# Optimization experiments

Measured on AMD Instinct MI355X. Metric: run time of the kernel, lower is better.

## Reference

```python
import jax, jax.numpy as jnp
import numpy as np

NUM_HEADS = 8

def _ln(x, w, b, eps=1e-5):
    m = x.mean(-1, keepdims=True)
    v = ((x - m) ** 2).mean(-1, keepdims=True)
    return (x - m) / jnp.sqrt(v + eps) * w + b

def _l2n(x, axis=-1, eps=1e-12):
    n = jnp.linalg.norm(x, axis=axis, keepdims=True)
    return x / jnp.maximum(n, eps)

def setup_inputs() -> dict:
    key = jax.random.key(0)
    ks = jax.random.split(key, 30)
    B, N, C, nc, t = 2, 4096, 256, 150, 3
    Hh = Ww = 64
    hid = 4 * C
    s = 0.02
    inp = {}
    inp['x'] = jax.random.normal(ks[0], (B, N, C), jnp.float32)
    inp['z'] = jax.random.normal(ks[1], (B, nc, (t + 1) * N), jnp.float32)
    inp['mem'] = jax.random.normal(ks[2], (B * t, N, C), jnp.float32)
    inp['clustering_w'] = s * jax.random.normal(ks[3], (nc, C), jnp.float32)
    inp['prompt1'] = jax.random.normal(ks[4], (nc,), jnp.float32)
    inp['tdt1'] = jnp.eye(nc, dtype=jnp.float32) + s * jax.random.normal(ks[5], (nc, nc), jnp.float32)
    inp['prompt2'] = jax.random.normal(ks[6], (nc,), jnp.float32)
    inp['tdt2'] = jnp.eye(nc, dtype=jnp.float32) + s * jax.random.normal(ks[7], (nc, nc), jnp.float32)
    inp['sim_alpha'] = jnp.ones((1,), jnp.float32)
    inp['sim_beta'] = jnp.zeros((1,), jnp.float32)
    inp['q_w'] = s * jax.random.normal(ks[8], (C, C), jnp.float32)
    inp['q_b'] = s * jax.random.normal(ks[9], (C,), jnp.float32)
    inp['k_w'] = s * jax.random.normal(ks[10], (C, C), jnp.float32)
    inp['k_b'] = s * jax.random.normal(ks[11], (C,), jnp.float32)
    inp['v_w'] = s * jax.random.normal(ks[12], (C, C), jnp.float32)
    inp['v_b'] = s * jax.random.normal(ks[13], (C,), jnp.float32)
    inp['proj_w'] = s * jax.random.normal(ks[14], (C, C), jnp.float32)
    inp['proj_b'] = s * jax.random.normal(ks[15], (C,), jnp.float32)
    inp['norm_w'] = jnp.ones((C,), jnp.float32)
    inp['norm_b'] = jnp.zeros((C,), jnp.float32)
    inp['fc1_w'] = s * jax.random.normal(ks[16], (hid, C), jnp.float32)
    inp['fc1_b'] = s * jax.random.normal(ks[17], (hid,), jnp.float32)
    inp['dw_w'] = s * jax.random.normal(ks[18], (hid, 1, 3, 3), jnp.float32)
    inp['dw_b'] = s * jax.random.normal(ks[19], (hid,), jnp.float32)
    inp['fc2_w'] = s * jax.random.normal(ks[20], (C, hid), jnp.float32)
    inp['fc2_b'] = s * jax.random.normal(ks[21], (C,), jnp.float32)
    inp['H'] = Hh
    inp['W'] = Ww
    inp['t'] = t
    return inp

def _forward(x, z, mem, clustering_w, prompt1, tdt1, prompt2, tdt2, sim_alpha, sim_beta,
             q_w, q_b, k_w, k_b, v_w, v_b, proj_w, proj_b, norm_w, norm_b,
             fc1_w, fc1_b, dw_w, dw_b, fc2_w, fc2_b, H, W, t):
    B, N, C = x.shape
    nc = clustering_w.shape[0]
    res = x
    T = t + 1
    # cat memory frames with current frame: [(B*T), N, C]
    xf = jnp.concatenate([mem.reshape(B, t, N, C), x[:, None]], axis=1).reshape(B * T, N, C)
    # clustering head: (SRPS approximated as identity) 1x1 conv dim->num_clusters
    cl = jnp.einsum('bnc,kc->bkn', xf, clustering_w)            # [(B*T), nc, N]
    cl = cl.reshape(B, T, nc, N).transpose(0, 2, 1, 3).reshape(B, nc, T * N)
    # top-down prompt modulation of z and cluster logits
    zc = z.transpose(0, 2, 1)                                   # [B, T*N, nc]
    cos = _l2n(zc, -1) @ _l2n(prompt1[None, :, None], axis=1)   # [B, T*N, 1]
    zc = (zc * jnp.clip(cos, 0.0, 1.0)) @ tdt1
    clc = cl.transpose(0, 2, 1)
    cos = _l2n(clc, -1) @ _l2n(prompt2[None, :, None], axis=1)
    clc = (clc * jnp.clip(cos, 0.0, 1.0)) @ tdt2
    cluster_x_z = ((clc + zc) * 0.5).transpose(0, 2, 1)          # [B, nc, T*N]
    # inner_center: per-frame soft assignment -> cluster centers
    center = cluster_x_z.reshape(B, nc, T, N).transpose(0, 2, 1, 3)  # [B, T, nc, N]
    assigned_results = center
    soft = jax.nn.softmax(center, axis=-1)
    cx = xf.reshape(B, T, N, C)
    cen = jnp.einsum('btkn,btnc->btkc', soft, cx)               # [B, T, nc, C]
    last, prev = cen[:, -1], cen[:, :-1]                        # [B,nc,C], [B,t,nc,C]
    dot = jnp.einsum('bkc,btkc->btk', last, prev)
    denom = jnp.maximum(jnp.linalg.norm(last, axis=-1)[:, None] * jnp.linalg.norm(prev, axis=-1), 1e-8)
    gate = jax.nn.sigmoid(sim_beta + sim_alpha * (dot / denom))  # [B, t, nc]
    C_in = last + (gate[..., None] * prev).sum(axis=1)          # [B, nc, C]
    C_in = _ln(C_in, norm_w, norm_b)
    # cross attention: tokens query cluster centers
    hd = C // NUM_HEADS
    q = (res @ q_w.T + q_b) * (1.0 / np.sqrt(hd))
    k = C_in @ k_w.T + k_b
    v = C_in @ v_w.T + v_b
    q = q.reshape(B, N, NUM_HEADS, hd).transpose(0, 2, 1, 3)
    k = k.reshape(B, nc, NUM_HEADS, hd).transpose(0, 2, 1, 3)
    v = v.reshape(B, nc, NUM_HEADS, hd).transpose(0, 2, 1, 3)
    attn = jax.nn.softmax(jnp.einsum('bhnd,bhkd->bhnk', q, k), axis=-1)
    o = jnp.einsum('bhnk,bhkd->bhnd', attn, v).transpose(0, 2, 1, 3).reshape(B, N, C)
    o = o @ proj_w.T + proj_b
    out = res + _ln(o, norm_w, norm_b)
    # MLP with depthwise conv
    h = out @ fc1_w.T + fc1_b                                   # [B, N, 4C]
    hid = h.shape[-1]
    h_img = h.transpose(0, 2, 1).reshape(B, hid, H, W)
    h_img = jax.lax.conv_general_dilated(h_img, dw_w, (1, 1), 'SAME',
                                         feature_group_count=hid,
                                         dimension_numbers=('NCHW', 'OIHW', 'NCHW'))
    h_img = h_img + dw_b[None, :, None, None]
    h = h_img.reshape(B, hid, N).transpose(0, 2, 1)
    h = jax.nn.gelu(h, approximate=False) @ fc2_w.T + fc2_b
    out = out + _ln(h, norm_w, norm_b)
    return out, cluster_x_z, assigned_results

def reference(x, z, mem, clustering_w, prompt1, tdt1, prompt2, tdt2, sim_alpha, sim_beta,
              q_w, q_b, k_w, k_b, v_w, v_b, proj_w, proj_b, norm_w, norm_b,
              fc1_w, fc1_b, dw_w, dw_b, fc2_w, fc2_b, H, W, t):
    return _forward(x, z, mem, clustering_w, prompt1, tdt1, prompt2, tdt2, sim_alpha, sim_beta,
                    q_w, q_b, k_w, k_b, v_w, v_b, proj_w, proj_b, norm_w, norm_b,
                    fc1_w, fc1_b, dw_w, dw_b, fc2_w, fc2_b, H, W, t)
```

## Files before the change

kernel.cpp:

```cpp
#include <hip/hip_runtime.h>
#include <math.h>


typedef __attribute__((ext_vector_type(8))) short bf16x8;
typedef __attribute__((ext_vector_type(4))) float f32x4;

__device__ __forceinline__ short f2b(float f) {
  union { float f; unsigned int u; } c; c.f = f;
  unsigned int r = (c.u + 0x7fffu + ((c.u >> 16) & 1u)) >> 16;
  return (short)r;
}

__device__ __forceinline__ float bred_sum(float v, float* red) {
  int tid = threadIdx.x;
  red[tid] = v; __syncthreads();
  #pragma unroll
  for (int s = 128; s > 0; s >>= 1) {
    if (tid < s) red[tid] += red[tid + s];
    __syncthreads();
  }
  float r = red[0]; __syncthreads();
  return r;
}

__global__ __launch_bounds__(256) void gemm_mfma(
    const float* __restrict__ A, const float* __restrict__ W,
    const float* __restrict__ bias, float* __restrict__ out,
    int M, int N, int K, float alpha)
{
  __shared__ __align__(16) short As[128 * 72];
  __shared__ __align__(16) short Bs[64 * 72];
  const int tid = threadIdx.x;
  const int m0 = blockIdx.x * 128;
  const int n0 = blockIdx.y * 64;
  const int wave = tid >> 6;
  const int lane = tid & 63;
  const int wm = wave & 1, wn = wave >> 1;
  const int t16 = lane & 15;
  const int k8 = (lane >> 4) * 8;

  f32x4 acc[4][2];
  #pragma unroll
  for (int i = 0; i < 4; ++i)
    #pragma unroll
    for (int j = 0; j < 2; ++j)
      acc[i][j] = (f32x4){0.f, 0.f, 0.f, 0.f};

  const int sr = tid >> 2;
  const int sk = (tid & 3) * 16;

  for (int k0 = 0; k0 < K; k0 += 64) {
    #pragma unroll
    for (int p = 0; p < 2; ++p) {
      const int row = sr + p * 64;
      const float* ap = &A[(size_t)(m0 + row) * K + k0 + sk];
      float4 v0 = *(const float4*)&ap[0];
      float4 v1 = *(const float4*)&ap[4];
      float4 v2 = *(const float4*)&ap[8];
      float4 v3 = *(const float4*)&ap[12];
      bf16x8 w0, w1;
      w0[0] = f2b(v0.x); w0[1] = f2b(v0.y); w0[2] = f2b(v0.z); w0[3] = f2b(v0.w);
      w0[4] = f2b(v1.x); w0[5] = f2b(v1.y); w0[6] = f2b(v1.z); w0[7] = f2b(v1.w);
      w1[0] = f2b(v2.x); w1[1] = f2b(v2.y); w1[2] = f2b(v2.z); w1[3] = f2b(v2.w);
      w1[4] = f2b(v3.x); w1[5] = f2b(v3.y); w1[6] = f2b(v3.z); w1[7] = f2b(v3.w);
      *(bf16x8*)&As[row * 72 + sk] = w0;
      *(bf16x8*)&As[row * 72 + sk + 8] = w1;
    }
    {
      const float* wp = &W[(size_t)(n0 + sr) * K + k0 + sk];
      float4 v0 = *(const float4*)&wp[0];
      float4 v1 = *(const float4*)&wp[4];
      float4 v2 = *(const float4*)&wp[8];
      float4 v3 = *(const float4*)&wp[12];
      bf16x8 w0, w1;
      w0[0] = f2b(v0.x); w0[1] = f2b(v0.y); w0[2] = f2b(v0.z); w0[3] = f2b(v0.w);
      w0[4] = f2b(v1.x); w0[5] = f2b(v1.y); w0[6] = f2b(v1.z); w0[7] = f2b(v1.w);
      w1[0] = f2b(v2.x); w1[1] = f2b(v2.y); w1[2] = f2b(v2.z); w1[3] = f2b(v2.w);
      w1[4] = f2b(v3.x); w1[5] = f2b(v3.y); w1[6] = f2b(v3.z); w1[7] = f2b(v3.w);
      *(bf16x8*)&Bs[sr * 72 + sk] = w0;
      *(bf16x8*)&Bs[sr * 72 + sk + 8] = w1;
    }
    __syncthreads();
    #pragma unroll
    for (int ks = 0; ks < 2; ++ks) {
      const int kofs = ks * 32 + k8;
      bf16x8 af0 = *(const bf16x8*)&As[(wm * 64 +  0 + t16) * 72 + kofs];
      bf16x8 af1 = *(const bf16x8*)&As[(wm * 64 + 16 + t16) * 72 + kofs];
      bf16x8 af2 = *(const bf16x8*)&As[(wm * 64 + 32 + t16) * 72 + kofs];
      bf16x8 af3 = *(const bf16x8*)&As[(wm * 64 + 48 + t16) * 72 + kofs];
      bf16x8 bf0 = *(const bf16x8*)&Bs[(wn * 32 +  0 + t16) * 72 + kofs];
      bf16x8 bf1 = *(const bf16x8*)&Bs[(wn * 32 + 16 + t16) * 72 + kofs];
      acc[0][0] = __builtin_amdgcn_mfma_f32_16x16x32_bf16(af0, bf0, acc[0][0], 0, 0, 0);
      acc[1][0] = __builtin_amdgcn_mfma_f32_16x16x32_bf16(af1, bf0, acc[1][0], 0, 0, 0);
      acc[2][0] = __builtin_amdgcn_mfma_f32_16x16x32_bf16(af2, bf0, acc[2][0], 0, 0, 0);
      acc[3][0] = __builtin_amdgcn_mfma_f32_16x16x32_bf16(af3, bf0, acc[3][0], 0, 0, 0);
      acc[0][1] = __builtin_amdgcn_mfma_f32_16x16x32_bf16(af0, bf1, acc[0][1], 0, 0, 0);
      acc[1][1] = __builtin_amdgcn_mfma_f32_16x16x32_bf16(af1, bf1, acc[1][1], 0, 0, 0);
      acc[2][1] = __builtin_amdgcn_mfma_f32_16x16x32_bf16(af2, bf1, acc[2][1], 0, 0, 0);
      acc[3][1] = __builtin_amdgcn_mfma_f32_16x16x32_bf16(af3, bf1, acc[3][1], 0, 0, 0);
    }
    __syncthreads();
  }
  const int r4 = (lane >> 4) * 4;
  #pragma unroll
  for (int ni = 0; ni < 2; ++ni) {
    const int gcol = n0 + wn * 32 + ni * 16 + t16;
    const float bb = bias[gcol];
    #pragma unroll
    for (int mi = 0; mi < 4; ++mi) {
      #pragma unroll
      for (int r = 0; r < 4; ++r) {
        const int gm = m0 + wm * 64 + mi * 16 + r4 + r;
        out[(size_t)gm * N + gcol] = alpha * (acc[mi][ni][r] + bb);
      }
    }
  }
}

__global__ __launch_bounds__(256) void prep_bt(
    const float* __restrict__ cw, const float* __restrict__ tdt2, const float* __restrict__ tdt1,
    short* __restrict__ cwb, short* __restrict__ TT)
{
  int idx = blockIdx.x * 256 + threadIdx.x;
  if (idx < 160 * 256) {
    int kc = idx >> 8, k = idx & 255;
    float v = (kc < 150) ? cw[kc * 256 + k] : 0.f;
    cwb[idx] = f2b(v);
  }
  if (idx < 160 * 320) {
    int kc = idx / 320, kk = idx - kc * 320;
    float t = 0.f;
    if (kc < 150) {
      if (kk < 150) t = tdt2[kk * 150 + kc];
      else if (kk >= 160 && kk < 310) t = tdt1[(kk - 160) * 150 + kc];
    }
    TT[idx] = f2b(t);
  }
}

__global__ __launch_bounds__(256) void xf_t(
    const float* __restrict__ x, const float* __restrict__ mem, short* __restrict__ xfT)
{
  __shared__ float tile[64][257];
  const int bt = blockIdx.y;
  const int n0 = blockIdx.x * 64;
  const int b = bt >> 2, ti = bt & 3;
  const float* xf = (ti < 3) ? (mem + (size_t)(b * 3 + ti) * 4096 * 256)
                             : (x + (size_t)b * 4096 * 256);
  const int tid = threadIdx.x;
  const int r = tid >> 2, cofs = (tid & 3) * 64;
  const float* src = xf + (size_t)(n0 + r) * 256 + cofs;
  #pragma unroll
  for (int i = 0; i < 16; ++i) {
    float4 v = *(const float4*)&src[i * 4];
    tile[r][cofs + i * 4 + 0] = v.x;
    tile[r][cofs + i * 4 + 1] = v.y;
    tile[r][cofs + i * 4 + 2] = v.z;
    tile[r][cofs + i * 4 + 3] = v.w;
  }
  __syncthreads();
  short* dst = xfT + ((size_t)bt * 256 + tid) * 4096 + n0;
  #pragma unroll
  for (int seg = 0; seg < 8; ++seg) {
    bf16x8 w;
    #pragma unroll
    for (int j = 0; j < 8; ++j) w[j] = f2b(tile[seg * 8 + j][tid]);
    *(bf16x8*)&dst[seg * 8] = w;
  }
}

__global__ __launch_bounds__(256) void fused_csz(
    const float* __restrict__ x, const float* __restrict__ mem, const float* __restrict__ z,
    const short* __restrict__ cwb, const short* __restrict__ TT,
    const float* __restrict__ p1, const float* __restrict__ p2,
    float* __restrict__ csz, float* __restrict__ asg)
{
  __shared__ __align__(16) short Acatile[64 * 328];
  __shared__ float p1s[160], p2s[160];
  __shared__ float sred[4][16][9];
  __shared__ float czs[64];
  const int tid = threadIdx.x;
  const int r0 = blockIdx.x * 64;
  const int b = r0 >> 14;
  const int mmg = r0 & 16383;
  const int ti = mmg >> 12, nn = mmg & 4095;
  const float* Ab = ((ti < 3) ? (mem + (size_t)(b * 3 + ti) * 4096 * 256)
                              : (x + (size_t)b * 4096 * 256)) + (size_t)nn * 256;
  const int wave = tid >> 6, lane = tid & 63;
  const int t16 = lane & 15, quad = lane >> 4, k8 = quad * 8;

  const int kr = tid >> 4, c4 = (tid & 15) * 4;
  float4 zv[10];
  #pragma unroll
  for (int it = 0; it < 10; ++it) {
    const int k = it * 16 + kr;
    zv[it] = make_float4(0.f, 0.f, 0.f, 0.f);
    if (k < 150) zv[it] = *(const float4*)&z[((size_t)b * 150 + k) * 16384 + mmg + c4];
  }
  if (tid < 160) {
    p2s[tid] = (tid < 150) ? p2[tid] : 0.f;
    p1s[tid] = (tid < 150) ? p1[tid] : 0.f;
  }

  f32x4 acc[10];
  #pragma unroll
  for (int i = 0; i < 10; ++i) acc[i] = (f32x4){0.f, 0.f, 0.f, 0.f};
  {
    const float* ap = Ab + (size_t)(wave * 16 + t16) * 256 + k8;
    const short* bp = cwb + t16 * 256 + k8;
    #pragma unroll 2
    for (int ks = 0; ks < 8; ++ks) {
      float4 v0 = *(const float4*)&ap[ks * 32];
      float4 v1 = *(const float4*)&ap[ks * 32 + 4];
      bf16x8 a;
      a[0] = f2b(v0.x); a[1] = f2b(v0.y); a[2] = f2b(v0.z); a[3] = f2b(v0.w);
      a[4] = f2b(v1.x); a[5] = f2b(v1.y); a[6] = f2b(v1.z); a[7] = f2b(v1.w);
      #pragma unroll
      for (int nf = 0; nf < 10; ++nf) {
        bf16x8 bv = *(const bf16x8*)&bp[nf * 4096 + ks * 32];
        acc[nf] = __builtin_amdgcn_mfma_f32_16x16x32_bf16(a, bv, acc[nf], 0, 0, 0);
      }
    }
  }
  __syncthreads();

  {
    float d[4] = {0.f, 0.f, 0.f, 0.f}, s[4] = {0.f, 0.f, 0.f, 0.f};
    float pn = 0.f;
    #pragma unroll
    for (int nf = 0; nf < 10; ++nf) {
      float a2 = p2s[nf * 16 + t16];
      pn += a2 * a2;
      #pragma unroll
      for (int r = 0; r < 4; ++r) {
        float v = acc[nf][r];
        d[r] = fmaf(v, a2, d[r]);
        s[r] = fmaf(v, v, s[r]);
      }
    }
    #pragma unroll
    for (int off = 1; off < 16; off <<= 1) {
      pn += __shfl_xor(pn, off);
      #pragma unroll
      for (int r = 0; r < 4; ++r) {
        d[r] += __shfl_xor(d[r], off);
        s[r] += __shfl_xor(s[r], off);
      }
    }
    const float spn = fmaxf(sqrtf(pn), 1e-12f);
    float cs[4];
    #pragma unroll
    for (int r = 0; r < 4; ++r) {
      float c = d[r] / (fmaxf(sqrtf(s[r]), 1e-12f) * spn);
      cs[r] = fminf(fmaxf(c, 0.f), 1.f);
    }
    #pragma unroll
    for (int nf = 0; nf < 10; ++nf)
      #pragma unroll
      for (int r = 0; r < 4; ++r)
        Acatile[(wave * 16 + quad * 4 + r) * 328 + nf * 16 + t16] = f2b(acc[nf][r] * cs[r]);
  }

  {
    float d[4] = {0.f, 0.f, 0.f, 0.f}, sv[4] = {0.f, 0.f, 0.f, 0.f};
    float pn = 0.f;
    #pragma unroll
    for (int it = 0; it < 10; ++it) {
      const int k = it * 16 + kr;
      const float a = p1s[k];
      d[0] = fmaf(zv[it].x, a, d[0]); d[1] = fmaf(zv[it].y, a, d[1]);
      d[2] = fmaf(zv[it].z, a, d[2]); d[3] = fmaf(zv[it].w, a, d[3]);
      sv[0] = fmaf(zv[it].x, zv[it].x, sv[0]); sv[1] = fmaf(zv[it].y, zv[it].y, sv[1]);
      sv[2] = fmaf(zv[it].z, zv[it].z, sv[2]); sv[3] = fmaf(zv[it].w, zv[it].w, sv[3]);
      pn = fmaf(a, a, pn);
    }
    #pragma unroll
    for (int off = 16; off < 64; off <<= 1) {
      pn += __shfl_xor(pn, off);
      #pragma unroll
      for (int r = 0; r < 4; ++r) {
        d[r] += __shfl_xor(d[r], off);
        sv[r] += __shfl_xor(sv[r], off);
      }
    }
    if ((lane >> 4) == 0) {
      #pragma unroll
      for (int r = 0; r < 4; ++r) {
        sred[wave][lane][r] = d[r];
        sred[wave][lane][4 + r] = sv[r];
      }
      sred[wave][lane][8] = pn;
    }
  }
  __syncthreads();
  if (tid < 64) {
    const int cg = tid >> 2, r = tid & 3;
    float dd = 0.f, ss = 0.f, pp = 0.f;
    #pragma unroll
    for (int w = 0; w < 4; ++w) {
      dd += sred[w][cg][r];
      ss += sred[w][cg][4 + r];
      pp += sred[w][cg][8];
    }
    float c = dd / (fmaxf(sqrtf(ss), 1e-12f) * fmaxf(sqrtf(pp), 1e-12f));
    czs[tid] = fminf(fmaxf(c, 0.f), 1.f);
  }
  __syncthreads();
  {
    const float cz0 = czs[c4 + 0], cz1 = czs[c4 + 1], cz2 = czs[c4 + 2], cz3 = czs[c4 + 3];
    #pragma unroll
    for (int it = 0; it < 10; ++it) {
      const int k = it * 16 + kr;
      Acatile[(c4 + 0) * 328 + 160 + k] = f2b(zv[it].x * cz0);
      Acatile[(c4 + 1) * 328 + 160 + k] = f2b(zv[it].y * cz1);
      Acatile[(c4 + 2) * 328 + 160 + k] = f2b(zv[it].z * cz2);
      Acatile[(c4 + 3) * 328 + 160 + k] = f2b(zv[it].w * cz3);
    }
  }
  __syncthreads();

  {
    const int wm = wave & 1, wn = wave >> 1;
    f32x4 c2[2][5];
    #pragma unroll
    for (int i = 0; i < 2; ++i)
      #pragma unroll
      for (int j = 0; j < 5; ++j)
        c2[i][j] = (f32x4){0.f, 0.f, 0.f, 0.f};
    const short* bp = TT + (size_t)(wn * 80 + t16) * 320 + k8;
    #pragma unroll 2
    for (int ks = 0; ks < 10; ++ks) {
      bf16x8 a0 = *(const bf16x8*)&Acatile[(wm * 32 + t16) * 328 + ks * 32 + k8];
      bf16x8 a1 = *(const bf16x8*)&Acatile[(wm * 32 + 16 + t16) * 328 + ks * 32 + k8];
      #pragma unroll
      for (int nf = 0; nf < 5; ++nf) {
        bf16x8 bv = *(const bf16x8*)&bp[nf * 5120 + ks * 32];
        c2[0][nf] = __builtin_amdgcn_mfma_f32_16x16x32_bf16(a0, bv, c2[0][nf], 0, 0, 0);
        c2[1][nf] = __builtin_amdgcn_mfma_f32_16x16x32_bf16(a1, bv, c2[1][nf], 0, 0, 0);
      }
    }
    #pragma unroll
    for (int nf = 0; nf < 5; ++nf) {
      const int kc = wn * 80 + nf * 16 + t16;
      if (kc < 150) {
        #pragma unroll
        for (int mf = 0; mf < 2; ++mf) {
          const int moff = wm * 32 + mf * 16 + quad * 4;
          float4 r4;
          r4.x = 0.5f * c2[mf][nf][0];
          r4.y = 0.5f * c2[mf][nf][1];
          r4.z = 0.5f * c2[mf][nf][2];
          r4.w = 0.5f * c2[mf][nf][3];
          *(float4*)&csz[((size_t)b * 150 + kc) * 16384 + mmg + moff] = r4;
          *(float4*)&asg[(((size_t)b * 4 + ti) * 150 + kc) * 4096 + nn + moff] = r4;
        }
      }
    }
  }
}

__global__ __launch_bounds__(256) void softmax_stats_e(
    const float* __restrict__ csz, float* __restrict__ lr_, short* __restrict__ ecsz)
{
  __shared__ float wred[8];
  const int row = blockIdx.x;
  const int bt = row / 150, k = row - bt * 150;
  const int b = bt >> 2, ti = bt & 3;
  const float* p = csz + ((size_t)b * 150 + k) * 16384 + ti * 4096;
  const int base = threadIdx.x * 16;
  float4 v[4];
  #pragma unroll
  for (int i = 0; i < 4; ++i) v[i] = *(const float4*)&p[base + i * 4];
  float mx = -1e30f;
  #pragma unroll
  for (int i = 0; i < 4; ++i)
    mx = fmaxf(mx, fmaxf(fmaxf(v[i].x, v[i].y), fmaxf(v[i].z, v[i].w)));
  #pragma unroll
  for (int off = 1; off < 64; off <<= 1) mx = fmaxf(mx, __shfl_xor(mx, off));
  const int wave = threadIdx.x >> 6, lane = threadIdx.x & 63;
  if (lane == 0) wred[wave] = mx;
  __syncthreads();
  mx = fmaxf(fmaxf(wred[0], wred[1]), fmaxf(wred[2], wred[3]));
  const float L = 1.4426950408889634f;
  float s = 0.f;
  bf16x8 e0, e1;
  #pragma unroll
  for (int i = 0; i < 2; ++i) {
    float a = exp2f((v[i].x - mx) * L);
    float bq = exp2f((v[i].y - mx) * L);
    float cq = exp2f((v[i].z - mx) * L);
    float dq = exp2f((v[i].w - mx) * L);
    s += a + bq + cq + dq;
    e0[i * 4 + 0] = f2b(a); e0[i * 4 + 1] = f2b(bq); e0[i * 4 + 2] = f2b(cq); e0[i * 4 + 3] = f2b(dq);
  }
  #pragma unroll
  for (int i = 2; i < 4; ++i) {
    float a = exp2f((v[i].x - mx) * L);
    float bq = exp2f((v[i].y - mx) * L);
    float cq = exp2f((v[i].z - mx) * L);
    float dq = exp2f((v[i].w - mx) * L);
    s += a + bq + cq + dq;
    e1[(i - 2) * 4 + 0] = f2b(a); e1[(i - 2) * 4 + 1] = f2b(bq);
    e1[(i - 2) * 4 + 2] = f2b(cq); e1[(i - 2) * 4 + 3] = f2b(dq);
  }
  #pragma unroll
  for (int off = 1; off < 64; off <<= 1) s += __shfl_xor(s, off);
  if (lane == 0) wred[4 + wave] = s;
  __syncthreads();
  short* er = ecsz + ((size_t)bt * 160 + k) * 4096 + base;
  *(bf16x8*)&er[0] = e0;
  *(bf16x8*)&er[8] = e1;
  if (threadIdx.x == 0) lr_[row] = wred[4] + wred[5] + wred[6] + wred[7];
}

__global__ __launch_bounds__(256) void gemm_cen_at(
    const short* __restrict__ ecsz, const short* __restrict__ xfT,
    float* __restrict__ cen)
{
  __shared__ __align__(16) short As[160 * 136];
  const int tid = threadIdx.x;
  const int chalf = blockIdx.x;
  const int bt = blockIdx.y;
  const int sp = blockIdx.z;
  const int n0 = sp * 128;
  const int wave = tid >> 6, lane = tid & 63;
  const int t16 = lane & 15, quad = lane >> 4, k8 = quad * 8;
  const int cbase = chalf * 128 + wave * 32;

  f32x4 acc[10][2];
  #pragma unroll
  for (int i = 0; i < 10; ++i) {
    acc[i][0] = (f32x4){0.f, 0.f, 0.f, 0.f};
    acc[i][1] = (f32x4){0.f, 0.f, 0.f, 0.f};
  }

  const short* erow = ecsz + (size_t)bt * 160 * 4096 + n0;
  #pragma unroll
  for (int p = 0; p < 10; ++p) {
    const int g = p * 256 + tid;
    const int row = g >> 4;
    const int col8 = (g & 15) * 8;
    *(bf16x8*)&As[row * 136 + col8] = *(const bf16x8*)&erow[(size_t)row * 4096 + col8];
  }
  __syncthreads();
  const short* xrow = xfT + (size_t)bt * 256 * 4096 + n0;
  #pragma unroll
  for (int kc = 0; kc < 4; ++kc) {
    bf16x8 b0 = *(const bf16x8*)&xrow[(size_t)(cbase + t16) * 4096 + kc * 32 + k8];
    bf16x8 b1 = *(const bf16x8*)&xrow[(size_t)(cbase + 16 + t16) * 4096 + kc * 32 + k8];
    #pragma unroll
    for (int mt = 0; mt < 10; ++mt) {
      bf16x8 aA = *(const bf16x8*)&As[(mt * 16 + t16) * 136 + kc * 32 + k8];
      acc[mt][0] = __builtin_amdgcn_mfma_f32_16x16x32_bf16(aA, b0, acc[mt][0], 0, 0, 0);
      acc[mt][1] = __builtin_amdgcn_mfma_f32_16x16x32_bf16(aA, b1, acc[mt][1], 0, 0, 0);
    }
  }
  #pragma unroll
  for (int mt = 0; mt < 10; ++mt) {
    #pragma unroll
    for (int r = 0; r < 4; ++r) {
      const int grow = mt * 16 + quad * 4 + r;
      if (grow < 150) {
        atomicAdd(&cen[((size_t)bt * 150 + grow) * 256 + cbase + t16], acc[mt][0][r]);
        atomicAdd(&cen[((size_t)bt * 150 + grow) * 256 + cbase + 16 + t16], acc[mt][1][r]);
      }
    }
  }
}

__global__ __launch_bounds__(256) void gate_ln(
    const float* __restrict__ cen, const float* __restrict__ lr_,
    const float* __restrict__ alpha_, const float* __restrict__ beta_,
    const float* __restrict__ nw, const float* __restrict__ nb, float* __restrict__ cin)
{
  __shared__ float red[256];
  int bk = blockIdx.x;
  int b = bk / 150, k = bk % 150;
  int c = threadIdx.x;
  const float* base = cen + ((size_t)b * 4 * 150) * 256;
  const float* lrb = lr_ + (size_t)b * 4 * 150;
  float lc  = base[((size_t)3 * 150 + k) * 256 + c] / lrb[3 * 150 + k];
  float p0  = base[((size_t)0 * 150 + k) * 256 + c] / lrb[0 * 150 + k];
  float p1v = base[((size_t)1 * 150 + k) * 256 + c] / lrb[1 * 150 + k];
  float p2v = base[((size_t)2 * 150 + k) * 256 + c] / lrb[2 * 150 + k];
  float nl = bred_sum(lc * lc, red);
  float q0 = bred_sum(p0 * p0, red);
  float q1 = bred_sum(p1v * p1v, red);
  float q2 = bred_sum(p2v * p2v, red);
  float d0 = bred_sum(lc * p0, red);
  float d1 = bred_sum(lc * p1v, red);
  float d2 = bred_sum(lc * p2v, red);
  float al = alpha_[0], be = beta_[0];
  float snl = sqrtf(nl);
  float g0 = 1.f / (1.f + expf(-(be + al * (d0 / fmaxf(snl * sqrtf(q0), 1e-8f)))));
  float g1 = 1.f / (1.f + expf(-(be + al * (d1 / fmaxf(snl * sqrtf(q1), 1e-8f)))));
  float g2 = 1.f / (1.f + expf(-(be + al * (d2 / fmaxf(snl * sqrtf(q2), 1e-8f)))));
  float ci = lc + g0 * p0 + g1 * p1v + g2 * p2v;
  float mu = bred_sum(ci, red) * (1.f / 256.f);
  float df = ci - mu;
  float var = bred_sum(df * df, red) * (1.f / 256.f);
  cin[(size_t)bk * 256 + c] = df * rsqrtf(var + 1e-5f) * nw[c] + nb[c];
}

__global__ __launch_bounds__(256) void gemm_nt(
    const float* __restrict__ A, const float* __restrict__ W,
    const float* __restrict__ bias, float* __restrict__ out,
    int M, int N, int K, float alpha)
{
  __shared__ __align__(16) float As[16][132];
  __shared__ __align__(16) float Ws[16][68];
  const int tid = threadIdx.x;
  const int m0 = blockIdx.x * 128;
  const int n0 = blockIdx.y * 64;
  const int tm = tid & 15;
  const int tn = tid >> 4;
  float acc[8][4];
  #pragma unroll
  for (int i = 0; i < 8; ++i)
    #pragma unroll
    for (int j = 0; j < 4; ++j) acc[i][j] = 0.f;

  const int lr = tid >> 2;
  const int lk = (tid & 3) * 4;

  for (int k0 = 0; k0 < K; k0 += 16) {
    #pragma unroll
    for (int p = 0; p < 2; ++p) {
      int r = lr + p * 64;
      int gm = m0 + r;
      float4 v = make_float4(0.f, 0.f, 0.f, 0.f);
      if (gm < M) v = *(const float4*)&A[(size_t)gm * K + k0 + lk];
      As[lk + 0][r] = v.x; As[lk + 1][r] = v.y; As[lk + 2][r] = v.z; As[lk + 3][r] = v.w;
    }
    {
      float4 v = *(const float4*)&W[(size_t)(n0 + lr) * K + k0 + lk];
      Ws[lk + 0][lr] = v.x; Ws[lk + 1][lr] = v.y; Ws[lk + 2][lr] = v.z; Ws[lk + 3][lr] = v.w;
    }
    __syncthreads();
    #pragma unroll
    for (int kk = 0; kk < 16; ++kk) {
      float4 a0 = *(const float4*)&As[kk][tm * 8];
      float4 a1 = *(const float4*)&As[kk][tm * 8 + 4];
      float4 w0 = *(const float4*)&Ws[kk][tn * 4];
      float av[8] = {a0.x, a0.y, a0.z, a0.w, a1.x, a1.y, a1.z, a1.w};
      float wv[4] = {w0.x, w0.y, w0.z, w0.w};
      #pragma unroll
      for (int i = 0; i < 8; ++i)
        #pragma unroll
        for (int j = 0; j < 4; ++j)
          acc[i][j] = fmaf(av[i], wv[j], acc[i][j]);
    }
    __syncthreads();
  }
  float4 bv = *(const float4*)&bias[n0 + tn * 4];
  float bb[4] = {bv.x, bv.y, bv.z, bv.w};
  #pragma unroll
  for (int i = 0; i < 8; ++i) {
    int gm = m0 + tm * 8 + i;
    if (gm >= M) continue;
    float4 r;
    r.x = alpha * (acc[i][0] + bb[0]);
    r.y = alpha * (acc[i][1] + bb[1]);
    r.z = alpha * (acc[i][2] + bb[2]);
    r.w = alpha * (acc[i][3] + bb[3]);
    *(float4*)&out[(size_t)gm * N + n0 + tn * 4] = r;
  }
}

__global__ __launch_bounds__(256) void attn_mfma(
    const float* __restrict__ q, const float* __restrict__ ks, const float* __restrict__ vs,
    float* __restrict__ o)
{
  __shared__ __align__(16) short Ps[128 * 168];
  __shared__ __align__(16) short VT[32 * 168];
  __shared__ float lrow[128];
  const int tid = threadIdx.x;
  const int bid = blockIdx.x;
  const int ntile = bid & 31;
  const int bh = bid >> 5;
  const int b = bh >> 3, h = bh & 7;
  const int n0 = ntile * 128;
  const int wave = tid >> 6, lane = tid & 63;
  const int t16 = lane & 15, quad = lane >> 4;
  const int k8 = quad * 8;
  const int wr = wave * 32;

  for (int i = tid; i < 5120; i += 256) {
    int d = i / 160, kc = i - d * 160;
    VT[d * 168 + kc] = (kc < 150) ? f2b(vs[((size_t)b * 150 + kc) * 256 + h * 32 + d]) : (short)0;
  }

  bf16x8 aQ[2];
  #pragma unroll
  for (int mt = 0; mt < 2; ++mt) {
    const float* qp = &q[((size_t)b * 4096 + n0 + wr + mt * 16 + t16) * 256 + h * 32 + k8];
    float4 v0 = *(const float4*)&qp[0];
    float4 v1 = *(const float4*)&qp[4];
    bf16x8 w;
    w[0] = f2b(v0.x); w[1] = f2b(v0.y); w[2] = f2b(v0.z); w[3] = f2b(v0.w);
    w[4] = f2b(v1.x); w[5] = f2b(v1.y); w[6] = f2b(v1.z); w[7] = f2b(v1.w);
    aQ[mt] = w;
  }

  f32x4 s[2][10];
  #pragma unroll
  for (int ct = 0; ct < 10; ++ct) {
    const int c = ct * 16 + t16;
    bf16x8 bK = {0, 0, 0, 0, 0, 0, 0, 0};
    if (c < 150) {
      const float* kp = &ks[((size_t)b * 150 + c) * 256 + h * 32 + k8];
      float4 v0 = *(const float4*)&kp[0];
      float4 v1 = *(const float4*)&kp[4];
      bK[0] = f2b(v0.x); bK[1] = f2b(v0.y); bK[2] = f2b(v0.z); bK[3] = f2b(v0.w);
      bK[4] = f2b(v1.x); bK[5] = f2b(v1.y); bK[6] = f2b(v1.z); bK[7] = f2b(v1.w);
    }
    f32x4 zero = (f32x4){0.f, 0.f, 0.f, 0.f};
    s[0][ct] = __builtin_amdgcn_mfma_f32_16x16x32_bf16(aQ[0], bK, zero, 0, 0, 0);
    s[1][ct] = __builtin_amdgcn_mfma_f32_16x16x32_bf16(aQ[1], bK, zero, 0, 0, 0);
  }

  #pragma unroll
  for (int mt = 0; mt < 2; ++mt) {
    #pragma unroll
    for (int r = 0; r < 4; ++r) {
      float mx = -1e30f;
      #pragma unroll
      for (int ct = 0; ct < 10; ++ct) {
        float v = s[mt][ct][r];
        if (ct == 9 && t16 >= 6) { v = -1e30f; s[mt][ct][r] = v; }
        mx = fmaxf(mx, v);
      }
      mx = fmaxf(mx, __shfl_xor(mx, 1));
      mx = fmaxf(mx, __shfl_xor(mx, 2));
      mx = fmaxf(mx, __shfl_xor(mx, 4));
      mx = fmaxf(mx, __shfl_xor(mx, 8));
      float ls = 0.f;
      #pragma unroll
      for (int ct = 0; ct < 10; ++ct) {
        float e = expf(s[mt][ct][r] - mx);
        s[mt][ct][r] = e;
        ls += e;
      }
      ls += __shfl_xor(ls, 1);
      ls += __shfl_xor(ls, 2);
      ls += __shfl_xor(ls, 4);
      ls += __shfl_xor(ls, 8);
      if (t16 == 0) lrow[wr + mt * 16 + quad * 4 + r] = 1.f / ls;
      #pragma unroll
      for (int ct = 0; ct < 10; ++ct)
        Ps[(wr + mt * 16 + quad * 4 + r) * 168 + ct * 16 + t16] = f2b(s[mt][ct][r]);
    }
  }
  __syncthreads();

  f32x4 oacc[2][2];
  #pragma unroll
  for (int i = 0; i < 2; ++i)
    #pragma unroll
    for (int j = 0; j < 2; ++j)
      oacc[i][j] = (f32x4){0.f, 0.f, 0.f, 0.f};
  #pragma unroll
  for (int kstep = 0; kstep < 5; ++kstep) {
    bf16x8 bV0 = *(const bf16x8*)&VT[( 0 + t16) * 168 + kstep * 32 + k8];
    bf16x8 bV1 = *(const bf16x8*)&VT[(16 + t16) * 168 + kstep * 32 + k8];
    #pragma unroll
    for (int mt = 0; mt < 2; ++mt) {
      bf16x8 aP = *(const bf16x8*)&Ps[(wr + mt * 16 + t16) * 168 + kstep * 32 + k8];
      oacc[mt][0] = __builtin_amdgcn_mfma_f32_16x16x32_bf16(aP, bV0, oacc[mt][0], 0, 0, 0);
      oacc[mt][1] = __builtin_amdgcn_mfma_f32_16x16x32_bf16(aP, bV1, oacc[mt][1], 0, 0, 0);
    }
  }
  #pragma unroll
  for (int mt = 0; mt < 2; ++mt) {
    #pragma unroll
    for (int nt = 0; nt < 2; ++nt) {
      const int d = nt * 16 + t16;
      #pragma unroll
      for (int r = 0; r < 4; ++r) {
        const int row = wr + mt * 16 + quad * 4 + r;
        o[((size_t)b * 4096 + n0 + row) * 256 + h * 32 + d] = oacc[mt][nt][r] * lrow[row];
      }
    }
  }
}

__global__ __launch_bounds__(256) void ln_res(
    const float* __restrict__ src, const float* __restrict__ res,
    const float* __restrict__ nw, const float* __restrict__ nb, float* __restrict__ dst)
{
  const int wave = threadIdx.x >> 6;
  const int lane = threadIdx.x & 63;
  const size_t row = (size_t)blockIdx.x * 4 + wave;
  const int c = lane * 4;
  float4 v = *(const float4*)&src[row * 256 + c];
  float s  = v.x + v.y + v.z + v.w;
  float s2 = v.x * v.x + v.y * v.y + v.z * v.z + v.w * v.w;
  #pragma unroll
  for (int off = 1; off < 64; off <<= 1) {
    s  += __shfl_xor(s, off);
    s2 += __shfl_xor(s2, off);
  }
  const float mu = s * (1.f / 256.f);
  const float var = s2 * (1.f / 256.f) - mu * mu;
  const float inv = rsqrtf(var + 1e-5f);
  float4 w = *(const float4*)&nw[c];
  float4 bb = *(const float4*)&nb[c];
  float4 rr = *(const float4*)&res[row * 256 + c];
  float4 d;
  d.x = rr.x + (v.x - mu) * inv * w.x + bb.x;
  d.y = rr.y + (v.y - mu) * inv * w.y + bb.y;
  d.z = rr.z + (v.z - mu) * inv * w.z + bb.z;
  d.w = rr.w + (v.w - mu) * inv * w.w + bb.w;
  *(float4*)&dst[row * 256 + c] = d;
}

__global__ __launch_bounds__(256) void conv_wt(
    const float* __restrict__ w, float* __restrict__ wt)
{
  int i = blockIdx.x * 256 + threadIdx.x;
  if (i < 9216) {
    int ch = i / 9, tap = i - ch * 9;
    wt[tap * 1024 + ch] = w[i];
  }
}

__global__ __launch_bounds__(256) void conv_gelu(
    const float* __restrict__ h, const float* __restrict__ wt, const float* __restrict__ bias,
    float* __restrict__ hc)
{
  const int pix = blockIdx.x;
  const int b = pix >> 12;
  const int n = pix & 4095;
  const int y = n >> 6, xx = n & 63;
  const int c4 = threadIdx.x * 4;
  float4 acc = *(const float4*)&bias[c4];
  const float* hb = h + ((size_t)b * 4096) * 1024 + c4;
  #pragma unroll
  for (int dy = 0; dy < 3; ++dy) {
    const int yy = y + dy - 1;
    if (yy < 0 || yy > 63) continue;
    #pragma unroll
    for (int dx = 0; dx < 3; ++dx) {
      const int xv = xx + dx - 1;
      if (xv < 0 || xv > 63) continue;
      float4 hv = *(const float4*)&hb[(size_t)(yy * 64 + xv) * 1024];
      float4 wv = *(const float4*)&wt[(dy * 3 + dx) * 1024 + c4];
      acc.x = fmaf(hv.x, wv.x, acc.x);
      acc.y = fmaf(hv.y, wv.y, acc.y);
      acc.z = fmaf(hv.z, wv.z, acc.z);
      acc.w = fmaf(hv.w, wv.w, acc.w);
    }
  }
  float4 g;
  g.x = 0.5f * acc.x * (1.f + erff(acc.x * 0.70710678118654752f));
  g.y = 0.5f * acc.y * (1.f + erff(acc.y * 0.70710678118654752f));
  g.z = 0.5f * acc.z * (1.f + erff(acc.z * 0.70710678118654752f));
  g.w = 0.5f * acc.w * (1.f + erff(acc.w * 0.70710678118654752f));
  *(float4*)&hc[((size_t)b * 4096 + n) * 1024 + c4] = g;
}

extern "C" void kernel_launch(void* const* d_in, const int* in_sizes, int n_in,
                              void* d_out, int out_size, void* d_ws, size_t ws_size,
                              hipStream_t stream)
{
  (void)in_sizes; (void)n_in; (void)out_size; (void)ws_size;
  const float* x    = (const float*)d_in[0];
  const float* z    = (const float*)d_in[1];
  const float* mem  = (const float*)d_in[2];
  const float* cw   = (const float*)d_in[3];
  const float* p1   = (const float*)d_in[4];
  const float* tdt1 = (const float*)d_in[5];
  const float* p2   = (const float*)d_in[6];
  const float* tdt2 = (const float*)d_in[7];
  const float* sal  = (const float*)d_in[8];
  const float* sbe  = (const float*)d_in[9];
  const float* q_w  = (const float*)d_in[10];
  const float* q_b  = (const float*)d_in[11];
  const float* k_w  = (const float*)d_in[12];
  const float* k_b  = (const float*)d_in[13];
  const float* v_w  = (const float*)d_in[14];
  const float* v_b  = (const float*)d_in[15];
  const float* pj_w = (const float*)d_in[16];
  const float* pj_b = (const float*)d_in[17];
  const float* nw   = (const float*)d_in[18];
  const float* nb   = (const float*)d_in[19];
  const float* f1w  = (const float*)d_in[20];
  const float* f1b  = (const float*)d_in[21];
  const float* dww  = (const float*)d_in[22];
  const float* dwb  = (const float*)d_in[23];
  const float* f2w  = (const float*)d_in[24];
  const float* f2b_ = (const float*)d_in[25];

  float* out = (float*)d_out;
  float* csz = out + 2097152;
  float* asg = csz + 4915200;

  float* ws    = (float*)d_ws;
  short* ecsz  = (short*)ws;
  short* TT    = (short*)(ws + 5242880);
  short* cwb   = (short*)(ws + 5275648);
  float* lr_   = ws + 5308416;
  float* cen   = ws + 5310816;
  float* cin   = ws + 5618016;
  float* q     = ws + 5694816;
  float* ksb   = ws + 7791968;
  float* vsb   = ws + 7868768;
  float* o     = ws + 7945568;
  short* xfT   = (short*)(ws + 10042720);
  float* h     = ws;
  float* hc    = ws + 8388608;
  float* tmp   = ws + 16777216;
  float* out1  = ws + 18874368;
  float* wt    = ws + 20971520;

  dim3 blk(256);
  prep_bt<<<dim3(200), blk, 0, stream>>>(cw, tdt2, tdt1, cwb, TT);
  xf_t<<<dim3(64, 8), blk, 0, stream>>>(x, mem, xfT);
  fused_csz<<<dim3(512), blk, 0, stream>>>(x, mem, z, cwb, TT, p1, p2, csz, asg);
  softmax_stats_e<<<dim3(1200), blk, 0, stream>>>(csz, lr_, ecsz);
  hipMemsetAsync(cen, 0, (size_t)1200 * 256 * sizeof(float), stream);
  gemm_cen_at<<<dim3(2, 8, 32), blk, 0, stream>>>(ecsz, xfT, cen);
  gate_ln<<<dim3(300), blk, 0, stream>>>(cen, lr_, sal, sbe, nw, nb, cin);
  gemm_mfma<<<dim3(64, 4), blk, 0, stream>>>(x, q_w, q_b, q, 8192, 256, 256, 0.17677669529663687f);
  gemm_nt<<<dim3(3, 4), blk, 0, stream>>>(cin, k_w, k_b, ksb, 300, 256, 256, 1.f);
  gemm_nt<<<dim3(3, 4), blk, 0, stream>>>(cin, v_w, v_b, vsb, 300, 256, 256, 1.f);
  attn_mfma<<<dim3(512), blk, 0, stream>>>(q, ksb, vsb, o);
  gemm_mfma<<<dim3(64, 4), blk, 0, stream>>>(o, pj_w, pj_b, tmp, 8192, 256, 256, 1.f);
  ln_res<<<dim3(2048), blk, 0, stream>>>(tmp, x, nw, nb, out1);
  gemm_mfma<<<dim3(64, 16), blk, 0, stream>>>(out1, f1w, f1b, h, 8192, 1024, 256, 1.f);
  conv_wt<<<dim3(36), blk, 0, stream>>>(dww, wt);
  conv_gelu<<<dim3(8192), blk, 0, stream>>>(h, wt, dwb, hc);
  gemm_mfma<<<dim3(64, 4), blk, 0, stream>>>(hc, f2w, f2b_, tmp, 8192, 256, 1024, 1.f);
  ln_res<<<dim3(2048), blk, 0, stream>>>(tmp, out1, nw, nb, out);
}
```

Measured before the change: 441.7 us.

## Halve row tiles in gemm_mfma and fused_csz to double block counts

The generic MFMA GEMM tile drops from 128x64 to 64x64, doubling its grid so the 8192-row GEMMs fill more compute units. fused_csz now handles 32 rows per block instead of 64 and splits the first GEMM's 160 cluster columns across wave pairs. That split needs a cross-wave shared-memory reduction for the cosine-similarity row sums, and the prompt norms are now computed by every thread straight from shared memory. The aim is better occupancy and latency hiding. The cost is lower per-block data reuse, so weight tiles are reloaded more often and the prompt-norm work is repeated.

```diff
diff --git a/kernel.cpp b/kernel.cpp
--- a/kernel.cpp
+++ b/kernel.cpp
@@ -28,10 +28,10 @@
     const float* __restrict__ bias, float* __restrict__ out,
     int M, int N, int K, float alpha)
 {
-  __shared__ __align__(16) short As[128 * 72];
+  __shared__ __align__(16) short As[64 * 72];
   __shared__ __align__(16) short Bs[64 * 72];
   const int tid = threadIdx.x;
-  const int m0 = blockIdx.x * 128;
+  const int m0 = blockIdx.x * 64;
   const int n0 = blockIdx.y * 64;
   const int wave = tid >> 6;
   const int lane = tid & 63;
@@ -39,9 +39,9 @@
   const int t16 = lane & 15;
   const int k8 = (lane >> 4) * 8;
 
-  f32x4 acc[4][2];
-  #pragma unroll
-  for (int i = 0; i < 4; ++i)
+  f32x4 acc[2][2];
+  #pragma unroll
+  for (int i = 0; i < 2; ++i)
     #pragma unroll
     for (int j = 0; j < 2; ++j)
       acc[i][j] = (f32x4){0.f, 0.f, 0.f, 0.f};
@@ -50,10 +50,8 @@
   const int sk = (tid & 3) * 16;
 
   for (int k0 = 0; k0 < K; k0 += 64) {
-    #pragma unroll
-    for (int p = 0; p < 2; ++p) {
-      const int row = sr + p * 64;
-      const float* ap = &A[(size_t)(m0 + row) * K + k0 + sk];
+    {
+      const float* ap = &A[(size_t)(m0 + sr) * K + k0 + sk];
       float4 v0 = *(const float4*)&ap[0];
       float4 v1 = *(const float4*)&ap[4];
       float4 v2 = *(const float4*)&ap[8];
@@ -63,8 +61,8 @@
       w0[4] = f2b(v1.x); w0[5] = f2b(v1.y); w0[6] = f2b(v1.z); w0[7] = f2b(v1.w);
       w1[0] = f2b(v2.x); w1[1] = f2b(v2.y); w1[2] = f2b(v2.z); w1[3] = f2b(v2.w);
       w1[4] = f2b(v3.x); w1[5] = f2b(v3.y); w1[6] = f2b(v3.z); w1[7] = f2b(v3.w);
-      *(bf16x8*)&As[row * 72 + sk] = w0;
-      *(bf16x8*)&As[row * 72 + sk + 8] = w1;
+      *(bf16x8*)&As[sr * 72 + sk] = w0;
+      *(bf16x8*)&As[sr * 72 + sk + 8] = w1;
     }
     {
       const float* wp = &W[(size_t)(n0 + sr) * K + k0 + sk];
@@ -84,20 +82,14 @@
     #pragma unroll
     for (int ks = 0; ks < 2; ++ks) {
       const int kofs = ks * 32 + k8;
-      bf16x8 af0 = *(const bf16x8*)&As[(wm * 64 +  0 + t16) * 72 + kofs];
-      bf16x8 af1 = *(const bf16x8*)&As[(wm * 64 + 16 + t16) * 72 + kofs];
-      bf16x8 af2 = *(const bf16x8*)&As[(wm * 64 + 32 + t16) * 72 + kofs];
-      bf16x8 af3 = *(const bf16x8*)&As[(wm * 64 + 48 + t16) * 72 + kofs];
+      bf16x8 af0 = *(const bf16x8*)&As[(wm * 32 +  0 + t16) * 72 + kofs];
+      bf16x8 af1 = *(const bf16x8*)&As[(wm * 32 + 16 + t16) * 72 + kofs];
       bf16x8 bf0 = *(const bf16x8*)&Bs[(wn * 32 +  0 + t16) * 72 + kofs];
       bf16x8 bf1 = *(const bf16x8*)&Bs[(wn * 32 + 16 + t16) * 72 + kofs];
       acc[0][0] = __builtin_amdgcn_mfma_f32_16x16x32_bf16(af0, bf0, acc[0][0], 0, 0, 0);
       acc[1][0] = __builtin_amdgcn_mfma_f32_16x16x32_bf16(af1, bf0, acc[1][0], 0, 0, 0);
-      acc[2][0] = __builtin_amdgcn_mfma_f32_16x16x32_bf16(af2, bf0, acc[2][0], 0, 0, 0);
-      acc[3][0] = __builtin_amdgcn_mfma_f32_16x16x32_bf16(af3, bf0, acc[3][0], 0, 0, 0);
       acc[0][1] = __builtin_amdgcn_mfma_f32_16x16x32_bf16(af0, bf1, acc[0][1], 0, 0, 0);
       acc[1][1] = __builtin_amdgcn_mfma_f32_16x16x32_bf16(af1, bf1, acc[1][1], 0, 0, 0);
-      acc[2][1] = __builtin_amdgcn_mfma_f32_16x16x32_bf16(af2, bf1, acc[2][1], 0, 0, 0);
-      acc[3][1] = __builtin_amdgcn_mfma_f32_16x16x32_bf16(af3, bf1, acc[3][1], 0, 0, 0);
     }
     __syncthreads();
   }
@@ -107,10 +99,10 @@
     const int gcol = n0 + wn * 32 + ni * 16 + t16;
     const float bb = bias[gcol];
     #pragma unroll
-    for (int mi = 0; mi < 4; ++mi) {
+    for (int mi = 0; mi < 2; ++mi) {
       #pragma unroll
       for (int r = 0; r < 4; ++r) {
-        const int gm = m0 + wm * 64 + mi * 16 + r4 + r;
+        const int gm = m0 + wm * 32 + mi * 16 + r4 + r;
         out[(size_t)gm * N + gcol] = alpha * (acc[mi][ni][r] + bb);
       }
     }
@@ -175,12 +167,13 @@
     const float* __restrict__ p1, const float* __restrict__ p2,
     float* __restrict__ csz, float* __restrict__ asg)
 {
-  __shared__ __align__(16) short Acatile[64 * 328];
-  __shared__ float p1s[160], p2s[160];
-  __shared__ float sred[4][16][9];
-  __shared__ float czs[64];
+  __shared__ __align__(16) short Acatile[32 * 328];
+  __shared__ __align__(16) float p1s[160], p2s[160];
+  __shared__ float sredA[32][2][2];
+  __shared__ float sredB[4][8][8];
+  __shared__ float czs[32];
   const int tid = threadIdx.x;
-  const int r0 = blockIdx.x * 64;
+  const int r0 = blockIdx.x * 32;
   const int b = r0 >> 14;
   const int mmg = r0 & 16383;
   const int ti = mmg >> 12, nn = mmg & 4095;
@@ -188,26 +181,28 @@
                               : (x + (size_t)b * 4096 * 256)) + (size_t)nn * 256;
   const int wave = tid >> 6, lane = tid & 63;
   const int t16 = lane & 15, quad = lane >> 4, k8 = quad * 8;
-
-  const int kr = tid >> 4, c4 = (tid & 15) * 4;
-  float4 zv[10];
-  #pragma unroll
-  for (int it = 0; it < 10; ++it) {
-    const int k = it * 16 + kr;
+  const int wm = wave & 1, wn = wave >> 1;
+
+  const int cidx = tid & 7, c4z = cidx * 4;
+  const int kr = tid >> 3;
+  float4 zv[5];
+  #pragma unroll
+  for (int it = 0; it < 5; ++it) {
+    const int k = it * 32 + kr;
     zv[it] = make_float4(0.f, 0.f, 0.f, 0.f);
-    if (k < 150) zv[it] = *(const float4*)&z[((size_t)b * 150 + k) * 16384 + mmg + c4];
+    if (k < 150) zv[it] = *(const float4*)&z[((size_t)b * 150 + k) * 16384 + mmg + c4z];
   }
   if (tid < 160) {
     p2s[tid] = (tid < 150) ? p2[tid] : 0.f;
     p1s[tid] = (tid < 150) ? p1[tid] : 0.f;
   }
 
-  f32x4 acc[10];
-  #pragma unroll
-  for (int i = 0; i < 10; ++i) acc[i] = (f32x4){0.f, 0.f, 0.f, 0.f};
+  f32x4 acc[5];
+  #pragma unroll
+  for (int i = 0; i < 5; ++i) acc[i] = (f32x4){0.f, 0.f, 0.f, 0.f};
   {
-    const float* ap = Ab + (size_t)(wave * 16 + t16) * 256 + k8;
-    const short* bp = cwb + t16 * 256 + k8;
+    const float* ap = Ab + (size_t)(wm * 16 + t16) * 256 + k8;
+    const short* bp = cwb + (size_t)(wn * 80 + t16) * 256 + k8;
     #pragma unroll 2
     for (int ks = 0; ks < 8; ++ks) {
       float4 v0 = *(const float4*)&ap[ks * 32];
@@ -216,7 +211,7 @@
       a[0] = f2b(v0.x); a[1] = f2b(v0.y); a[2] = f2b(v0.z); a[3] = f2b(v0.w);
       a[4] = f2b(v1.x); a[5] = f2b(v1.y); a[6] = f2b(v1.z); a[7] = f2b(v1.w);
       #pragma unroll
-      for (int nf = 0; nf < 10; ++nf) {
+      for (int nf = 0; nf < 5; ++nf) {
         bf16x8 bv = *(const bf16x8*)&bp[nf * 4096 + ks * 32];
         acc[nf] = __builtin_amdgcn_mfma_f32_16x16x32_bf16(a, bv, acc[nf], 0, 0, 0);
       }
@@ -224,13 +219,23 @@
   }
   __syncthreads();
 
+  float pn1 = 0.f, pn2 = 0.f;
+  {
+    const float4* q1 = (const float4*)p1s;
+    const float4* q2 = (const float4*)p2s;
+    #pragma unroll
+    for (int i = 0; i < 40; ++i) {
+      float4 a1 = q1[i], a2 = q2[i];
+      pn1 += a1.x * a1.x + a1.y * a1.y + a1.z * a1.z + a1.w * a1.w;
+      pn2 += a2.x * a2.x + a2.y * a2.y + a2.z * a2.z + a2.w * a2.w;
+    }
+  }
+
   {
     float d[4] = {0.f, 0.f, 0.f, 0.f}, s[4] = {0.f, 0.f, 0.f, 0.f};
-    float pn = 0.f;
-    #pragma unroll
-    for (int nf = 0; nf < 10; ++nf) {
-      float a2 = p2s[nf * 16 + t16];
-      pn += a2 * a2;
+    #pragma unroll
+    for (int nf = 0; nf < 5; ++nf) {
+      float a2 = p2s[wn * 80 + nf * 16 + t16];
       #pragma unroll
       for (int r = 0; r < 4; ++r) {
         float v = acc[nf][r];
@@ -240,120 +245,119 @@
     }
     #pragma unroll
     for (int off = 1; off < 16; off <<= 1) {
-      pn += __shfl_xor(pn, off);
       #pragma unroll
       for (int r = 0; r < 4; ++r) {
         d[r] += __shfl_xor(d[r], off);
         s[r] += __shfl_xor(s[r], off);
       }
     }
-    const float spn = fmaxf(sqrtf(pn), 1e-12f);
-    float cs[4];
-    #pragma unroll
-    for (int r = 0; r < 4; ++r) {
-      float c = d[r] / (fmaxf(sqrtf(s[r]), 1e-12f) * spn);
-      cs[r] = fminf(fmaxf(c, 0.f), 1.f);
-    }
-    #pragma unroll
-    for (int nf = 0; nf < 10; ++nf)
-      #pragma unroll
-      for (int r = 0; r < 4; ++r)
-        Acatile[(wave * 16 + quad * 4 + r) * 328 + nf * 16 + t16] = f2b(acc[nf][r] * cs[r]);
+    if (t16 == 0) {
+      #pragma unroll
+      for (int r = 0; r < 4; ++r) {
+        sredA[wm * 16 + quad * 4 + r][wn][0] = d[r];
+        sredA[wm * 16 + quad * 4 + r][wn][1] = s[r];
+      }
+    }
   }
 
   {
     float d[4] = {0.f, 0.f, 0.f, 0.f}, sv[4] = {0.f, 0.f, 0.f, 0.f};
-    float pn = 0.f;
-    #pragma unroll
-    for (int it = 0; it < 10; ++it) {
-      const int k = it * 16 + kr;
+    #pragma unroll
+    for (int it = 0; it < 5; ++it) {
+      const int k = it * 32 + kr;
       const float a = p1s[k];
       d[0] = fmaf(zv[it].x, a, d[0]); d[1] = fmaf(zv[it].y, a, d[1]);
       d[2] = fmaf(zv[it].z, a, d[2]); d[3] = fmaf(zv[it].w, a, d[3]);
       sv[0] = fmaf(zv[it].x, zv[it].x, sv[0]); sv[1] = fmaf(zv[it].y, zv[it].y, sv[1]);
       sv[2] = fmaf(zv[it].z, zv[it].z, sv[2]); sv[3] = fmaf(zv[it].w, zv[it].w, sv[3]);
-      pn = fmaf(a, a, pn);
-    }
-    #pragma unroll
-    for (int off = 16; off < 64; off <<= 1) {
-      pn += __shfl_xor(pn, off);
+    }
+    #pragma unroll
+    for (int off = 8; off < 64; off <<= 1) {
       #pragma unroll
       for (int r = 0; r < 4; ++r) {
         d[r] += __shfl_xor(d[r], off);
         sv[r] += __shfl_xor(sv[r], off);
       }
     }
-    if ((lane >> 4) == 0) {
+    if (lane < 8) {
       #pragma unroll
       for (int r = 0; r < 4; ++r) {
-        sred[wave][lane][r] = d[r];
-        sred[wave][lane][4 + r] = sv[r];
-      }
-      sred[wave][lane][8] = pn;
+        sredB[wave][lane][r] = d[r];
+        sredB[wave][lane][4 + r] = sv[r];
+      }
     }
   }
   __syncthreads();
-  if (tid < 64) {
+
+  {
+    const float spn2 = fmaxf(sqrtf(pn2), 1e-12f);
+    float cs[4];
+    #pragma unroll
+    for (int r = 0; r < 4; ++r) {
+      const int row = wm * 16 + quad * 4 + r;
+      float dd = sredA[row][0][0] + sredA[row][1][0];
+      float ss = sredA[row][0][1] + sredA[row][1][1];
+      float c = dd / (fmaxf(sqrtf(ss), 1e-12f) * spn2);
+      cs[r] = fminf(fmaxf(c, 0.f), 1.f);
+    }
+    #pragma unroll
+    for (int nf = 0; nf < 5; ++nf)
+      #pragma unroll
+      for (int r = 0; r < 4; ++r)
+        Acatile[(wm * 16 + quad * 4 + r) * 328 + wn * 80 + nf * 16 + t16] = f2b(acc[nf][r] * cs[r]);
+  }
+  if (tid < 32) {
     const int cg = tid >> 2, r = tid & 3;
-    float dd = 0.f, ss = 0.f, pp = 0.f;
+    float dd = 0.f, ss = 0.f;
     #pragma unroll
     for (int w = 0; w < 4; ++w) {
-      dd += sred[w][cg][r];
-      ss += sred[w][cg][4 + r];
-      pp += sred[w][cg][8];
-    }
-    float c = dd / (fmaxf(sqrtf(ss), 1e-12f) * fmaxf(sqrtf(pp), 1e-12f));
+      dd += sredB[w][cg][r];
+      ss += sredB[w][cg][4 + r];
+    }
+    float c = dd / (fmaxf(sqrtf(ss), 1e-12f) * fmaxf(sqrtf(pn1), 1e-12f));
     czs[tid] = fminf(fmaxf(c, 0.f), 1.f);
   }
   __syncthreads();
+
   {
-    const float cz0 = czs[c4 + 0], cz1 = czs[c4 + 1], cz2 = czs[c4 + 2], cz3 = czs[c4 + 3];
-    #pragma unroll
-    for (int it = 0; it < 10; ++it) {
-      const int k = it * 16 + kr;
-      Acatile[(c4 + 0) * 328 + 160 + k] = f2b(zv[it].x * cz0);
-      Acatile[(c4 + 1) * 328 + 160 + k] = f2b(zv[it].y * cz1);
-      Acatile[(c4 + 2) * 328 + 160 + k] = f2b(zv[it].z * cz2);
-      Acatile[(c4 + 3) * 328 + 160 + k] = f2b(zv[it].w * cz3);
+    const float cz0 = czs[c4z + 0], cz1 = czs[c4z + 1], cz2 = czs[c4z + 2], cz3 = czs[c4z + 3];
+    #pragma unroll
+    for (int it = 0; it < 5; ++it) {
+      const int k = it * 32 + kr;
+      Acatile[(c4z + 0) * 328 + 160 + k] = f2b(zv[it].x * cz0);
+      Acatile[(c4z + 1) * 328 + 160 + k] = f2b(zv[it].y * cz1);
+      Acatile[(c4z + 2) * 328 + 160 + k] = f2b(zv[it].z * cz2);
+      Acatile[(c4z + 3) * 328 + 160 + k] = f2b(zv[it].w * cz3);
     }
   }
   __syncthreads();
 
   {
-    const int wm = wave & 1, wn = wave >> 1;
-    f32x4 c2[2][5];
-    #pragma unroll
-    for (int i = 0; i < 2; ++i)
-      #pragma unroll
-      for (int j = 0; j < 5; ++j)
-        c2[i][j] = (f32x4){0.f, 0.f, 0.f, 0.f};
+    f32x4 c2[5];
+    #pragma unroll
+    for (int j = 0; j < 5; ++j) c2[j] = (f32x4){0.f, 0.f, 0.f, 0.f};
     const short* bp = TT + (size_t)(wn * 80 + t16) * 320 + k8;
     #pragma unroll 2
     for (int ks = 0; ks < 10; ++ks) {
-      bf16x8 a0 = *(const bf16x8*)&Acatile[(wm * 32 + t16) * 328 + ks * 32 + k8];
-      bf16x8 a1 = *(const bf16x8*)&Acatile[(wm * 32 + 16 + t16) * 328 + ks * 32 + k8];
+      bf16x8 a0 = *(const bf16x8*)&Acatile[(wm * 16 + t16) * 328 + ks * 32 + k8];
       #pragma unroll
       for (int nf = 0; nf < 5; ++nf) {
         bf16x8 bv = *(const bf16x8*)&bp[nf * 5120 + ks * 32];
-        c2[0][nf] = __builtin_amdgcn_mfma_f32_16x16x32_bf16(a0, bv, c2[0][nf], 0, 0, 0);
-        c2[1][nf] = __builtin_amdgcn_mfma_f32_16x16x32_bf16(a1, bv, c2[1][nf], 0, 0, 0);
+        c2[nf] = __builtin_amdgcn_mfma_f32_16x16x32_bf16(a0, bv, c2[nf], 0, 0, 0);
       }
     }
     #pragma unroll
     for (int nf = 0; nf < 5; ++nf) {
       const int kc = wn * 80 + nf * 16 + t16;
       if (kc < 150) {
-        #pragma unroll
-        for (int mf = 0; mf < 2; ++mf) {
-          const int moff = wm * 32 + mf * 16 + quad * 4;
-          float4 r4;
-          r4.x = 0.5f * c2[mf][nf][0];
-          r4.y = 0.5f * c2[mf][nf][1];
-          r4.z = 0.5f * c2[mf][nf][2];
-          r4.w = 0.5f * c2[mf][nf][3];
-          *(float4*)&csz[((size_t)b * 150 + kc) * 16384 + mmg + moff] = r4;
-          *(float4*)&asg[(((size_t)b * 4 + ti) * 150 + kc) * 4096 + nn + moff] = r4;
-        }
+        const int moff = wm * 16 + quad * 4;
+        float4 r4;
+        r4.x = 0.5f * c2[nf][0];
+        r4.y = 0.5f * c2[nf][1];
+        r4.z = 0.5f * c2[nf][2];
+        r4.w = 0.5f * c2[nf][3];
+        *(float4*)&csz[((size_t)b * 150 + kc) * 16384 + mmg + moff] = r4;
+        *(float4*)&asg[(((size_t)b * 4 + ti) * 150 + kc) * 4096 + nn + moff] = r4;
       }
     }
   }
@@ -816,20 +820,20 @@
   dim3 blk(256);
   prep_bt<<<dim3(200), blk, 0, stream>>>(cw, tdt2, tdt1, cwb, TT);
   xf_t<<<dim3(64, 8), blk, 0, stream>>>(x, mem, xfT);
-  fused_csz<<<dim3(512), blk, 0, stream>>>(x, mem, z, cwb, TT, p1, p2, csz, asg);
+  fused_csz<<<dim3(1024), blk, 0, stream>>>(x, mem, z, cwb, TT, p1, p2, csz, asg);
   softmax_stats_e<<<dim3(1200), blk, 0, stream>>>(csz, lr_, ecsz);
   hipMemsetAsync(cen, 0, (size_t)1200 * 256 * sizeof(float), stream);
   gemm_cen_at<<<dim3(2, 8, 32), blk, 0, stream>>>(ecsz, xfT, cen);
   gate_ln<<<dim3(300), blk, 0, stream>>>(cen, lr_, sal, sbe, nw, nb, cin);
-  gemm_mfma<<<dim3(64, 4), blk, 0, stream>>>(x, q_w, q_b, q, 8192, 256, 256, 0.17677669529663687f);
+  gemm_mfma<<<dim3(128, 4), blk, 0, stream>>>(x, q_w, q_b, q, 8192, 256, 256, 0.17677669529663687f);
   gemm_nt<<<dim3(3, 4), blk, 0, stream>>>(cin, k_w, k_b, ksb, 300, 256, 256, 1.f);
   gemm_nt<<<dim3(3, 4), blk, 0, stream>>>(cin, v_w, v_b, vsb, 300, 256, 256, 1.f);
   attn_mfma<<<dim3(512), blk, 0, stream>>>(q, ksb, vsb, o);
-  gemm_mfma<<<dim3(64, 4), blk, 0, stream>>>(o, pj_w, pj_b, tmp, 8192, 256, 256, 1.f);
+  gemm_mfma<<<dim3(128, 4), blk, 0, stream>>>(o, pj_w, pj_b, tmp, 8192, 256, 256, 1.f);
   ln_res<<<dim3(2048), blk, 0, stream>>>(tmp, x, nw, nb, out1);
-  gemm_mfma<<<dim3(64, 16), blk, 0, stream>>>(out1, f1w, f1b, h, 8192, 1024, 256, 1.f);
+  gemm_mfma<<<dim3(128, 16), blk, 0, stream>>>(out1, f1w, f1b, h, 8192, 1024, 256, 1.f);
   conv_wt<<<dim3(36), blk, 0, stream>>>(dww, wt);
   conv_gelu<<<dim3(8192), blk, 0, stream>>>(h, wt, dwb, hc);
-  gemm_mfma<<<dim3(64, 4), blk, 0, stream>>>(hc, f2w, f2b_, tmp, 8192, 256, 1024, 1.f);
+  gemm_mfma<<<dim3(128, 4), blk, 0, stream>>>(hc, f2w, f2b_, tmp, 8192, 256, 1024, 1.f);
   ln_res<<<dim3(2048), blk, 0, stream>>>(tmp, out1, nw, nb, out);
 }
```

Result: slower. 467.0 us (+5.7%).
